# Optimization experiments

Measured on AMD Instinct MI355X. Metric: run time of the kernel, lower is better.

The kernel has to match this reference:

```python
import jax, jax.numpy as jnp
import numpy as np
from jax import lax

B, T, H, C = 64, 512, 1024, 8


def setup_inputs() -> dict:
    key = jax.random.key(0)
    ks = jax.random.split(key, 7)
    encoding = jax.random.normal(ks[0], (B, T, H), dtype=jnp.float32)
    labels = jax.random.randint(ks[1], (B, 3 * T), 0, C)
    W = jax.random.normal(ks[2], (3, C, H), dtype=jnp.float32) * 0.02
    b = jax.random.normal(ks[3], (3, C), dtype=jnp.float32) * 0.02
    start_trans = jax.random.normal(ks[4], (3, C), dtype=jnp.float32) * 0.1
    end_trans = jax.random.normal(ks[5], (3, C), dtype=jnp.float32) * 0.1
    trans = jax.random.normal(ks[6], (3, C, C), dtype=jnp.float32) * 0.1
    return {"encoding": encoding, "labels": labels, "W": W, "b": b,
            "start_trans": start_trans, "end_trans": end_trans, "trans": trans}


def crf_neg_log_lik(em, tags, start, end, trans):
    # em [B,T,C], tags [B,T] -> scalar (torchcrf reduction='sum', loss = -llh)
    bsz = em.shape[0]
    # numerator: score of gold path
    em_sc = jnp.take_along_axis(em, tags[:, :, None], axis=2)[..., 0].sum(axis=1)
    tr_sc = trans[tags[:, :-1], tags[:, 1:]].sum(axis=1)
    num = start[tags[:, 0]] + em_sc + tr_sc + end[tags[:, -1]]
    # denominator: forward algorithm (log partition)
    a0 = start[None, :] + em[:, 0]  # [B,C]

    def step(a, e_t):
        a_new = jax.nn.logsumexp(a[:, :, None] + trans[None] + e_t[:, None, :], axis=1)
        return a_new, None

    aT, _ = lax.scan(step, a0, jnp.moveaxis(em[:, 1:], 1, 0))
    logZ = jax.nn.logsumexp(aT + end[None, :], axis=1)
    return -(num - logZ).sum()


def viterbi(em, start, end, trans):
    # em [B,T,C] -> best tag path [B,T] (no mask: all sequences full length)
    v0 = start[None, :] + em[:, 0]

    def step(v, e_t):
        s = v[:, :, None] + trans[None]          # [B,C_prev,C_cur]
        bp = jnp.argmax(s, axis=1)               # [B,C]
        return jnp.max(s, axis=1) + e_t, bp

    vT, bps = lax.scan(step, v0, jnp.moveaxis(em[:, 1:], 1, 0))  # bps [T-1,B,C]
    last = jnp.argmax(vT + end[None, :], axis=1)  # [B]

    def back(tag, bp):
        prev = jnp.take_along_axis(bp, tag[:, None], axis=1)[:, 0]
        return prev, prev

    _, rev = lax.scan(back, last, bps, reverse=True)  # [T-1,B], tags for t=0..T-2
    tags = jnp.concatenate([rev, last[None]], axis=0)  # [T,B]
    return tags.T


def reference(encoding, labels, W, b, start_trans, end_trans, trans):
    # three per-task projections: logits [3,B,T,C]
    logits = jnp.einsum('bth,kch->kbtc', encoding, W) + b[:, None, None, :]
    tags = jnp.stack(jnp.split(labels, 3, axis=1))  # [3,B,T] (task/process/material)
    losses = jax.vmap(crf_neg_log_lik)(logits, tags, start_trans, end_trans, trans)
    loss = losses.sum()
    pred = jax.vmap(viterbi)(logits, start_trans, end_trans, trans)  # [3,B,T]
    return loss, logits, pred
```

## Files before the change

kernel.cpp:

```cpp
#include <hip/hip_runtime.h>

#define NB 64
#define NT 512
#define NH 1024
#define NC 8
#define NK 3
#define BT (NB*NT)
#define LOGITS_N (NK*BT*NC)

typedef unsigned short ushort;
typedef unsigned int uint;
typedef __attribute__((ext_vector_type(8))) short short8v;
typedef __attribute__((ext_vector_type(4))) float float4v;
union S8 { short8v v; ushort u[8]; };

#define QP1  0xB1
#define QP2  0x4E
#define ROR4 0x124
#define ROR8 0x128
#define HM   0x141

template<int CTRL>
__device__ __forceinline__ float dppf(float x) {
  return __int_as_float(__builtin_amdgcn_update_dpp(0, __float_as_int(x), CTRL, 0xF, 0xF, true));
}
template<int CTRL>
__device__ __forceinline__ int dppi(int x) {
  return __builtin_amdgcn_update_dpp(0, x, CTRL, 0xF, 0xF, true);
}

__device__ __forceinline__ void gload_lds16(const void* g, void* l) {
  __builtin_amdgcn_global_load_lds(
      (const __attribute__((address_space(1))) void*)g,
      (__attribute__((address_space(3))) void*)l, 16, 0, 0);
}

__global__ __launch_bounds__(256) void init_kernel(const float* __restrict__ W,
                                                   ushort* __restrict__ WB,
                                                   float* __restrict__ out) {
  const int i = blockIdx.x * 256 + threadIdx.x;
  const int ci = i >> 11;
  const int rem = i & 2047;
  const int q = rem >> 9;
  const int l = (rem >> 3) & 63;
  const int e = i & 7;
  const int k = ci * 64 + (q >> 1) * 32 + ((l >> 4) << 3) + e;
  const int j = (q & 1) * 16 + (l & 15);
  float v = 0.0f;
  if (j < 24) v = W[(j >> 3) * (NC * NH) + (j & 7) * NH + k];
  const uint b = __float_as_uint(v);
  const ushort h1 = (ushort)(b >> 16);
  const float f1 = __uint_as_float(b & 0xFFFF0000u);
  const float r1 = v - f1;
  const uint b2 = __float_as_uint(r1);
  const ushort h2 = (ushort)(b2 >> 16);
  const float f2 = __uint_as_float(b2 & 0xFFFF0000u);
  const float r2 = r1 - f2;
  const ushort h3 = (ushort)(__float_as_uint(r2) >> 16);
  WB[i] = h1;
  WB[32768 + i] = h2;
  WB[65536 + i] = h3;
  if (i == 0) out[0] = 0.0f;
}

__global__ __launch_bounds__(256, 2) void proj_kernel(const float* __restrict__ enc,
                                                      const ushort* __restrict__ WB,
                                                      const float* __restrict__ bias,
                                                      float* __restrict__ out) {
  __shared__ float  sA[2][4096];
  __shared__ ushort sB[2][6144];
  const int tid = threadIdx.x;
  const int lane = tid & 63;
  const int w = tid >> 6;
  const int row0 = blockIdx.x * 64;
  const int chrot = blockIdx.x & 15;
  const float* eb = enc + (size_t)row0 * 1024;

  float4v acc0 = {0.0f, 0.0f, 0.0f, 0.0f};
  float4v acc1 = {0.0f, 0.0f, 0.0f, 0.0f};

  auto stageA = [&](int cx, int buf) {
#pragma unroll
    for (int i = 0; i < 4; ++i) {
      const int rbase = w * 16 + i * 4;
      const int r = rbase + (lane >> 4);
      const int s = (lane & 15) ^ (r & 15);
      gload_lds16(eb + (size_t)r * 1024 + cx * 64 + s * 4, &sA[buf][rbase * 64]);
    }
  };
  auto stageB = [&](int cx, int buf) {
#pragma unroll
    for (int i = 0; i < 3; ++i) {
      const int u = i * 4 + w;
      gload_lds16(WB + i * 32768 + cx * 2048 + w * 512 + lane * 8,
                  &sB[buf][u * 512]);
    }
  };

  auto compute = [&](int buf) {
    const float* ar = &sA[buf][(w * 16 + (lane & 15)) * 64];
    const ushort* sBf = &sB[buf][0];
    const int rx = lane & 15;
    const int g = lane >> 4;
#pragma unroll
    for (int kkb = 0; kkb < 2; ++kkb) {
      const int s0 = kkb * 8 + g * 2;
      const float4 e0 = *(const float4*)&ar[(s0 ^ rx) * 4];
      const float4 e1 = *(const float4*)&ar[((s0 + 1) ^ rx) * 4];
      S8 a1, a2, a3;
      const float vals[8] = {e0.x, e0.y, e0.z, e0.w, e1.x, e1.y, e1.z, e1.w};
#pragma unroll
      for (int t = 0; t < 8; ++t) {
        const float v = vals[t];
        const uint b = __float_as_uint(v);
        a1.u[t] = (ushort)(b >> 16);
        const float f1 = __uint_as_float(b & 0xFFFF0000u);
        const float r1 = v - f1;
        const uint b2 = __float_as_uint(r1);
        a2.u[t] = (ushort)(b2 >> 16);
        const float f2 = __uint_as_float(b2 & 0xFFFF0000u);
        const float r2 = r1 - f2;
        a3.u[t] = (ushort)(__float_as_uint(r2) >> 16);
      }
#pragma unroll
      for (int jt = 0; jt < 2; ++jt) {
        const int q = kkb * 2 + jt;
        const short8v w1 = *(const short8v*)&sBf[0 * 2048 + q * 512 + lane * 8];
        const short8v w2 = *(const short8v*)&sBf[1 * 2048 + q * 512 + lane * 8];
        const short8v w3 = *(const short8v*)&sBf[2 * 2048 + q * 512 + lane * 8];
        float4v acc = jt ? acc1 : acc0;
        acc = __builtin_amdgcn_mfma_f32_16x16x32_bf16(a1.v, w1, acc, 0, 0, 0);
        acc = __builtin_amdgcn_mfma_f32_16x16x32_bf16(a2.v, w1, acc, 0, 0, 0);
        acc = __builtin_amdgcn_mfma_f32_16x16x32_bf16(a1.v, w2, acc, 0, 0, 0);
        acc = __builtin_amdgcn_mfma_f32_16x16x32_bf16(a2.v, w2, acc, 0, 0, 0);
        acc = __builtin_amdgcn_mfma_f32_16x16x32_bf16(a3.v, w1, acc, 0, 0, 0);
        acc = __builtin_amdgcn_mfma_f32_16x16x32_bf16(a1.v, w3, acc, 0, 0, 0);
        if (jt) acc1 = acc; else acc0 = acc;
      }
    }
  };

  stageA(chrot, 0);
  stageB(chrot, 0);
  __syncthreads();

#pragma unroll 1
  for (int t = 0; t < 16; ++t) {
    const int buf = t & 1;
    if (t < 15) {
      const int cx = (t + 1) ^ chrot;
      stageA(cx, buf ^ 1);
      stageB(cx, buf ^ 1);
    }
    compute(buf);
    __syncthreads();
  }

  const int g = lane >> 4, cx2 = lane & 15;
#pragma unroll
  for (int jt = 0; jt < 2; ++jt) {
    const int j = jt * 16 + cx2;
    if (j < 24) {
      const float bj = bias[j];
      const float4v acc = jt ? acc1 : acc0;
      float* ob = out + 1 + (size_t)(j >> 3) * (BT * 8) + (j & 7);
#pragma unroll
      for (int qq = 0; qq < 4; ++qq) {
        const int grow = row0 + w * 16 + g * 4 + qq;
        ob[(size_t)grow * 8] = acc[qq] + bj;
      }
    }
  }
}

__global__ __launch_bounds__(512) void crf_kernel(const int* __restrict__ labels,
                                                  const float* __restrict__ startT,
                                                  const float* __restrict__ endT,
                                                  const float* __restrict__ trans,
                                                  float* __restrict__ d_out) {
  __shared__ float sA[32 * 64];
  __shared__ float sVB[32 * 8];
  __shared__ int   sBP[512];
  __shared__ int   sMap[32 * 8];
  __shared__ int   sEnt[32];
  __shared__ float sRed[32];
  __shared__ unsigned char sTags[512];
  __shared__ int sTerm;

  const int tid = threadIdx.x;
  const int lane = tid & 63;
  const int w = tid >> 6;
  const int c = lane & 7;
  const int p = (lane >> 3) & 7;
  const int role = (blockIdx.x >= 192);
  const int seq = role ? blockIdx.x - 192 : blockIdx.x;
  const int k = seq >> 6, b = seq & 63;
  const float* em = d_out + 1 + ((size_t)k * BT + (size_t)b * 512) * 8;
  const float* trk = trans + k * 64;
  const int* lab = labels + b * (NK * NT) + k * NT;

  float Txc[8];
#pragma unroll
  for (int kk = 0; kk < 8; ++kk) Txc[kk] = trk[(c ^ kk) * 8 + c];
  const float Tpc = trk[p * 8 + c];
  const float startc = startT[k * 8 + c];
  const float endc = endT[k * 8 + c];

  if (!role) {
    float Mxc[8];
#pragma unroll
    for (int kk = 0; kk < 8; ++kk) Mxc[kk] = __expf(Txc[kk]);

#pragma unroll 1
    for (int it = 0; it < 4; ++it) {
      const int i = w * 4 + it;
      const int t0 = i * 16;
      const int te = (t0 + 16 < 512) ? (t0 + 16) : 511;
      float EX[16];
      EX[0] = em[(t0 + 1) * 8 + c];
#pragma unroll
      for (int j = 1; j < 16; ++j) {
        int t = t0 + 1 + j;
        EX[j] = (t <= te) ? __expf(em[t * 8 + c]) : 1.0f;
      }
      float V = __expf(Tpc + EX[0]);
#pragma unroll
      for (int j = 1; j < 16; ++j) {
        int t = t0 + 1 + j;
        if (t <= te) {
          float x1 = dppf<QP1>(V), x2 = dppf<QP2>(V), x3 = dppf<QP2>(x1);
          float x7 = dppf<HM>(V), x6 = dppf<QP1>(x7), x5 = dppf<QP2>(x7), x4 = dppf<QP2>(x6);
          float s01 = fmaf(x1, Mxc[1], V * Mxc[0]);
          float s23 = fmaf(x3, Mxc[3], x2 * Mxc[2]);
          float s45 = fmaf(x5, Mxc[5], x4 * Mxc[4]);
          float s67 = fmaf(x7, Mxc[7], x6 * Mxc[6]);
          V = ((s01 + s23) + (s45 + s67)) * EX[j];
        }
        if (j == 8) V *= 0x1p-32f;
      }
      sA[i * 64 + lane] = V;
    }
    __syncthreads();

    float logZ = 0.0f;
    if (w == 0) {
      float al = __expf(startc + em[c]);
      float lz = 0.0f;
#pragma unroll 1
      for (int i = 0; i < 32; ++i) {
        const float* Ai = &sA[i * 64];
        float A0 = Ai[(c ^ 0) * 8 + c], A1 = Ai[(c ^ 1) * 8 + c];
        float A2 = Ai[(c ^ 2) * 8 + c], A3 = Ai[(c ^ 3) * 8 + c];
        float A4 = Ai[(c ^ 4) * 8 + c], A5 = Ai[(c ^ 5) * 8 + c];
        float A6 = Ai[(c ^ 6) * 8 + c], A7 = Ai[(c ^ 7) * 8 + c];
        float a1 = dppf<QP1>(al), a2 = dppf<QP2>(al), a3 = dppf<QP2>(a1);
        float a4 = dppf<ROR4>(al), a5 = dppf<ROR4>(a1), a6 = dppf<ROR4>(a2), a7 = dppf<ROR4>(a3);
        float s01 = fmaf(a1, A1, al * A0);
        float s23 = fmaf(a3, A3, a2 * A2);
        float s45 = fmaf(a5, A5, a4 * A4);
        float s67 = fmaf(a7, A7, a6 * A6);
        float s = (s01 + s23) + (s45 + s67);
        float ss = s;
        ss += dppf<QP1>(ss); ss += dppf<QP2>(ss); ss += dppf<ROR4>(ss);
        lz += __logf(ss);
        al = s * (1.0f / ss);
      }
      float se = al * __expf(endc);
      se += dppf<QP1>(se); se += dppf<QP2>(se); se += dppf<ROR4>(se);
      logZ = lz + __logf(se) + 1024.0f * 0.69314718055994531f;
    } else {
      int idx = (w - 1) * 64 + lane;
      float ns = 0.0f;
      {
        int tg = lab[idx];
        ns += em[(size_t)idx * 8 + tg] + trk[tg * 8 + lab[idx + 1]];
      }
      if (idx < 64) {
        int t = idx + 448;
        int tg = lab[t];
        ns += em[(size_t)t * 8 + tg];
        if (t < 511) ns += trk[tg * 8 + lab[t + 1]];
      }
      ns += dppf<QP1>(ns); ns += dppf<QP2>(ns); ns += dppf<HM>(ns); ns += dppf<ROR8>(ns);
      if ((lane & 15) == 0) sRed[(w - 1) * 4 + (lane >> 4)] = ns;
    }
    __syncthreads();
    if (tid == 0) {
      float num = startT[k * 8 + lab[0]] + endT[k * 8 + lab[511]];
#pragma unroll
      for (int u = 0; u < 28; ++u) num += sRed[u];
      atomicAdd(d_out, logZ - num);
    }
  } else {
#pragma unroll 1
    for (int it = 0; it < 4; ++it) {
      const int i = w * 4 + it;
      const int t0 = i * 16;
      const int te = (t0 + 16 < 512) ? (t0 + 16) : 511;
      float emv[16];
#pragma unroll
      for (int j = 0; j < 16; ++j) {
        int t = t0 + 1 + j;
        emv[j] = (t <= te) ? em[t * 8 + c] : 0.0f;
      }
      float V = Tpc + emv[0];
#pragma unroll
      for (int j = 1; j < 16; ++j) {
        int t = t0 + 1 + j;
        if (t <= te) {
          float x1 = dppf<QP1>(V), x2 = dppf<QP2>(V), x3 = dppf<QP2>(x1);
          float x7 = dppf<HM>(V), x6 = dppf<QP1>(x7), x5 = dppf<QP2>(x7), x4 = dppf<QP2>(x6);
          float c0 = V + Txc[0], c1 = x1 + Txc[1], c2 = x2 + Txc[2], c3 = x3 + Txc[3];
          float c4 = x4 + Txc[4], c5 = x5 + Txc[5], c6 = x6 + Txc[6], c7 = x7 + Txc[7];
          float m0 = fmaxf(fmaxf(c0, c1), c2);
          float m1 = fmaxf(fmaxf(c3, c4), c5);
          float m2 = fmaxf(c6, c7);
          V = fmaxf(fmaxf(m0, m1), m2) + emv[j];
        }
      }
      sA[i * 64 + lane] = V;
    }
    __syncthreads();

    if (w == 0) {
      float v = startc + em[c];
#pragma unroll 1
      for (int i = 0; i < 32; ++i) {
        if (lane < 8) sVB[i * 8 + c] = v;
        const float* Ai = &sA[i * 64];
        float A0 = Ai[(c ^ 0) * 8 + c], A1 = Ai[(c ^ 1) * 8 + c];
        float A2 = Ai[(c ^ 2) * 8 + c], A3 = Ai[(c ^ 3) * 8 + c];
        float A4 = Ai[(c ^ 4) * 8 + c], A5 = Ai[(c ^ 5) * 8 + c];
        float A6 = Ai[(c ^ 6) * 8 + c], A7 = Ai[(c ^ 7) * 8 + c];
        float a1 = dppf<QP1>(v), a2 = dppf<QP2>(v), a3 = dppf<QP2>(a1);
        float a4 = dppf<ROR4>(v), a5 = dppf<ROR4>(a1), a6 = dppf<ROR4>(a2), a7 = dppf<ROR4>(a3);
        float c0 = v + A0, c1 = a1 + A1, c2 = a2 + A2, c3 = a3 + A3;
        float c4 = a4 + A4, c5 = a5 + A5, c6 = a6 + A6, c7 = a7 + A7;
        float m0 = fmaxf(fmaxf(c0, c1), c2);
        float m1 = fmaxf(fmaxf(c3, c4), c5);
        float m2 = fmaxf(c6, c7);
        v = fmaxf(fmaxf(m0, m1), m2);
      }
      float lv = v + endc;
      int li = c;
      {
        float ov; int oi; bool take;
        ov = dppf<QP1>(lv); oi = dppi<QP1>(li);
        take = (ov > lv) || (ov == lv && oi < li); lv = take ? ov : lv; li = take ? oi : li;
        ov = dppf<QP2>(lv); oi = dppi<QP2>(li);
        take = (ov > lv) || (ov == lv && oi < li); lv = take ? ov : lv; li = take ? oi : li;
        ov = dppf<ROR4>(lv); oi = dppi<ROR4>(li);
        take = (ov > lv) || (ov == lv && oi < li); lv = take ? ov : lv; li = take ? oi : li;
      }
      if (lane == 0) sTerm = li;
    }
    __syncthreads();

    if (w < 4) {
      const int u = lane >> 3;
      const int i = w * 8 + u;
      const int t0 = i * 16;
      const int te = (t0 + 16 < 512) ? (t0 + 16) : 511;
      float emv[16];
#pragma unroll
      for (int j = 0; j < 16; ++j) {
        int t = t0 + 1 + j;
        emv[j] = (t <= te) ? em[t * 8 + c] : 0.0f;
      }
      float v = sVB[i * 8 + c];
#pragma unroll
      for (int j = 0; j < 16; ++j) {
        int t = t0 + 1 + j;
        if (t <= te) {
          float x1 = dppf<QP1>(v), x2 = dppf<QP2>(v), x3 = dppf<QP2>(x1);
          float x7 = dppf<HM>(v), x6 = dppf<QP1>(x7), x5 = dppf<QP2>(x7), x4 = dppf<QP2>(x6);
          float c0 = v + Txc[0], c1 = x1 + Txc[1], c2 = x2 + Txc[2], c3 = x3 + Txc[3];
          float c4 = x4 + Txc[4], c5 = x5 + Txc[5], c6 = x6 + Txc[6], c7 = x7 + Txc[7];
          float m0 = fmaxf(fmaxf(c0, c1), c2);
          float m1 = fmaxf(fmaxf(c3, c4), c5);
          float m2 = fmaxf(c6, c7);
          float best = fmaxf(fmaxf(m0, m1), m2);
          int a0 = (c0 == best) ? (c ^ 0) : 8;
          int a1i = (c1 == best) ? (c ^ 1) : 8;
          int a2i = (c2 == best) ? (c ^ 2) : 8;
          int a3i = (c3 == best) ? (c ^ 3) : 8;
          int a4i = (c4 == best) ? (c ^ 4) : 8;
          int a5i = (c5 == best) ? (c ^ 5) : 8;
          int a6i = (c6 == best) ? (c ^ 6) : 8;
          int a7i = (c7 == best) ? (c ^ 7) : 8;
          int arg = min(min(min(a0, a1i), min(a2i, a3i)),
                        min(min(a4i, a5i), min(a6i, a7i)));
          v = best + emv[j];
          int wd = arg << (3 * c);
          wd |= dppi<QP1>(wd); wd |= dppi<QP2>(wd); wd |= dppi<HM>(wd);
          if ((lane & 7) == 0) sBP[t] = wd;
        }
      }
    }
    __syncthreads();

    if (w < 4) {
      const int u = lane >> 3;
      const int i = w * 8 + u;
      const int t0 = i * 16;
      const int te = (t0 + 16 < 512) ? (t0 + 16) : 511;
      int tag = c;
#pragma unroll
      for (int j = 16; j >= 1; --j) {
        int t = t0 + j;
        if (t <= te) tag = (sBP[t] >> (3 * tag)) & 7;
      }
      sMap[i * 8 + c] = tag;
    }
    __syncthreads();
    if (tid == 0) {
      int cur = sTerm;
#pragma unroll 1
      for (int i = 31; i >= 0; --i) { cur = sMap[i * 8 + cur]; sEnt[i] = cur; }
    }
    __syncthreads();
    if (w == 0 && lane < 32) {
      const int i = lane;
      const int t0 = i * 16;
      const int te = (t0 + 16 < 512) ? (t0 + 16) : 511;
      int tag = (i == 31) ? sTerm : sEnt[i + 1];
      if (i == 31) sTags[511] = (unsigned char)tag;
#pragma unroll
      for (int j = 16; j >= 1; --j) {
        int t = t0 + j;
        if (t <= te) { tag = (sBP[t] >> (3 * tag)) & 7; sTags[t - 1] = (unsigned char)tag; }
      }
    }
    __syncthreads();
    float* outp = d_out + 1 + LOGITS_N + (size_t)seq * 512;
    outp[tid] = (float)sTags[tid];
  }
}

extern "C" void kernel_launch(void* const* d_in, const int* in_sizes, int n_in,
                              void* d_out, int out_size, void* d_ws, size_t ws_size,
                              hipStream_t stream) {
  const float* enc    = (const float*)d_in[0];
  const int*   labels = (const int*)  d_in[1];
  const float* W      = (const float*)d_in[2];
  const float* bias   = (const float*)d_in[3];
  const float* startT = (const float*)d_in[4];
  const float* endT   = (const float*)d_in[5];
  const float* trans  = (const float*)d_in[6];
  float* out = (float*)d_out;
  ushort* WB = (ushort*)d_ws;

  init_kernel<<<dim3(128), dim3(256), 0, stream>>>(W, WB, out);
  proj_kernel<<<dim3(512), dim3(256), 0, stream>>>(enc, WB, bias, out);
  crf_kernel<<<dim3(384), dim3(512), 0, stream>>>(labels, startT, endT, trans, out);
}
```

Before: 227.3 us.

## Triple-buffer encoding tiles and use counted vmcnt waits for deeper prefetch

The projection kernel's encoding tile staging moves from double to triple buffering, so A loads run two iterations ahead while weight tiles stay one ahead. Full __syncthreads waits are replaced by explicit s_waitcnt vmcnt counts plus raw barriers, so only the loads needed for the current tile must land before compute starts. This aims to hide more global-load latency behind the MFMA work. In exchange it uses more LDS per block (which may affect the two-blocks-per-CU target) and depends on hand-counted outstanding-load numbers being correct.

```diff
diff --git a/kernel.cpp b/kernel.cpp
--- a/kernel.cpp
+++ b/kernel.cpp
@@ -67,7 +67,7 @@
                                                       const ushort* __restrict__ WB,
                                                       const float* __restrict__ bias,
                                                       float* __restrict__ out) {
-  __shared__ float  sA[2][4096];
+  __shared__ float  sA[3][4096];
   __shared__ ushort sB[2][6144];
   const int tid = threadIdx.x;
   const int lane = tid & 63;
@@ -79,27 +79,31 @@
   float4v acc0 = {0.0f, 0.0f, 0.0f, 0.0f};
   float4v acc1 = {0.0f, 0.0f, 0.0f, 0.0f};
 
-  auto stageA = [&](int cx, int buf) {
+  auto stageA = [&](int t) {
+    const int cx = t ^ chrot;
+    float* dst = &sA[t % 3][0];
 #pragma unroll
     for (int i = 0; i < 4; ++i) {
       const int rbase = w * 16 + i * 4;
       const int r = rbase + (lane >> 4);
       const int s = (lane & 15) ^ (r & 15);
-      gload_lds16(eb + (size_t)r * 1024 + cx * 64 + s * 4, &sA[buf][rbase * 64]);
+      gload_lds16(eb + (size_t)r * 1024 + cx * 64 + s * 4, &dst[rbase * 64]);
     }
   };
-  auto stageB = [&](int cx, int buf) {
+  auto stageB = [&](int t) {
+    const int cx = t ^ chrot;
+    ushort* dst = &sB[t & 1][0];
 #pragma unroll
     for (int i = 0; i < 3; ++i) {
       const int u = i * 4 + w;
       gload_lds16(WB + i * 32768 + cx * 2048 + w * 512 + lane * 8,
-                  &sB[buf][u * 512]);
+                  &dst[u * 512]);
     }
   };
 
-  auto compute = [&](int buf) {
-    const float* ar = &sA[buf][(w * 16 + (lane & 15)) * 64];
-    const ushort* sBf = &sB[buf][0];
+  auto compute = [&](int abuf, int bbuf) {
+    const float* ar = &sA[abuf][(w * 16 + (lane & 15)) * 64];
+    const ushort* sBf = &sB[bbuf][0];
     const int rx = lane & 15;
     const int g = lane >> 4;
 #pragma unroll
@@ -140,20 +144,22 @@
     }
   };
 
-  stageA(chrot, 0);
-  stageB(chrot, 0);
-  __syncthreads();
+  stageA(0);
+  stageB(0);
+  stageA(1);
 
 #pragma unroll 1
   for (int t = 0; t < 16; ++t) {
-    const int buf = t & 1;
-    if (t < 15) {
-      const int cx = (t + 1) ^ chrot;
-      stageA(cx, buf ^ 1);
-      stageB(cx, buf ^ 1);
-    }
-    compute(buf);
-    __syncthreads();
+    if (t + 1 < 16) stageB(t + 1);
+    if (t + 2 < 16) stageA(t + 2);
+    if (t < 14)       asm volatile("s_waitcnt vmcnt(11)" ::: "memory");
+    else if (t == 14) asm volatile("s_waitcnt vmcnt(7)" ::: "memory");
+    else              asm volatile("s_waitcnt vmcnt(0)" ::: "memory");
+    __builtin_amdgcn_s_barrier();
+    asm volatile("" ::: "memory");
+    compute(t % 3, t & 1);
+    asm volatile("" ::: "memory");
+    __builtin_amdgcn_s_barrier();
   }
 
   const int g = lane >> 4, cx2 = lane & 15;
```

New measurement: 226.2 us. Within noise of the previous version (-0.5%).

## Split K across waves in projection kernel with register-resident weight fragments

Applied to the files above, without the earlier changes.

The projection kernel now gives each wave a quarter of the K dimension for all 64 rows. Before, each wave owned 16 rows over the full K. Each wave holds its 12 bf16 weight fragments in registers and reuses them across four row groups. Weights are staged once per K-quarter instead of once per 64-column chunk. Partial accumulators are reduced across waves through shared memory before the bias add and store. This adds registers for four accumulator pairs and an LDS reduction epilogue, which may lower occupancy, and it drops the per-block chunk rotation.

```diff
diff --git a/kernel.cpp b/kernel.cpp
--- a/kernel.cpp
+++ b/kernel.cpp
@@ -67,107 +67,134 @@
                                                       const ushort* __restrict__ WB,
                                                       const float* __restrict__ bias,
                                                       float* __restrict__ out) {
-  __shared__ float  sA[2][4096];
-  __shared__ ushort sB[2][6144];
+  __shared__ float smem[20480];
+  float* const sAf = smem;
+  ushort* const sBu = (ushort*)(smem + 8192);
   const int tid = threadIdx.x;
   const int lane = tid & 63;
   const int w = tid >> 6;
   const int row0 = blockIdx.x * 64;
-  const int chrot = blockIdx.x & 15;
   const float* eb = enc + (size_t)row0 * 1024;
 
-  float4v acc0 = {0.0f, 0.0f, 0.0f, 0.0f};
-  float4v acc1 = {0.0f, 0.0f, 0.0f, 0.0f};
-
-  auto stageA = [&](int cx, int buf) {
+  float4v acc[4][2];
+#pragma unroll
+  for (int rg = 0; rg < 4; ++rg)
+#pragma unroll
+    for (int jt = 0; jt < 2; ++jt) acc[rg][jt] = (float4v){0.f, 0.f, 0.f, 0.f};
+
+  auto stageA = [&](int kqN, int rgN, int bufN) {
 #pragma unroll
     for (int i = 0; i < 4; ++i) {
-      const int rbase = w * 16 + i * 4;
-      const int r = rbase + (lane >> 4);
-      const int s = (lane & 15) ^ (r & 15);
-      gload_lds16(eb + (size_t)r * 1024 + cx * 64 + s * 4, &sA[buf][rbase * 64]);
+      const int r = w * 4 + i;
+      gload_lds16(eb + (size_t)(rgN * 16 + r) * 1024 + kqN * 256 + (lane ^ r) * 4,
+                  &sAf[bufN * 4096 + r * 256]);
     }
   };
-  auto stageB = [&](int cx, int buf) {
-#pragma unroll
-    for (int i = 0; i < 3; ++i) {
-      const int u = i * 4 + w;
-      gload_lds16(WB + i * 32768 + cx * 2048 + w * 512 + lane * 8,
-                  &sB[buf][u * 512]);
+  auto stageB = [&](int kqN) {
+    const int ci = kqN * 4 + w;
+#pragma unroll
+    for (int i = 0; i < 12; ++i) {
+      const int sp = i >> 2, q = i & 3;
+      gload_lds16(WB + sp * 32768 + ci * 2048 + q * 512 + lane * 8,
+                  &sBu[w * 6144 + sp * 2048 + q * 512]);
     }
   };
 
-  auto compute = [&](int buf) {
-    const float* ar = &sA[buf][(w * 16 + (lane & 15)) * 64];
-    const ushort* sBf = &sB[buf][0];
-    const int rx = lane & 15;
-    const int g = lane >> 4;
-#pragma unroll
-    for (int kkb = 0; kkb < 2; ++kkb) {
-      const int s0 = kkb * 8 + g * 2;
-      const float4 e0 = *(const float4*)&ar[(s0 ^ rx) * 4];
-      const float4 e1 = *(const float4*)&ar[((s0 + 1) ^ rx) * 4];
-      S8 a1, a2, a3;
-      const float vals[8] = {e0.x, e0.y, e0.z, e0.w, e1.x, e1.y, e1.z, e1.w};
-#pragma unroll
-      for (int t = 0; t < 8; ++t) {
-        const float v = vals[t];
-        const uint b = __float_as_uint(v);
-        a1.u[t] = (ushort)(b >> 16);
-        const float f1 = __uint_as_float(b & 0xFFFF0000u);
-        const float r1 = v - f1;
-        const uint b2 = __float_as_uint(r1);
-        a2.u[t] = (ushort)(b2 >> 16);
-        const float f2 = __uint_as_float(b2 & 0xFFFF0000u);
-        const float r2 = r1 - f2;
-        a3.u[t] = (ushort)(__float_as_uint(r2) >> 16);
-      }
-#pragma unroll
-      for (int jt = 0; jt < 2; ++jt) {
-        const int q = kkb * 2 + jt;
-        const short8v w1 = *(const short8v*)&sBf[0 * 2048 + q * 512 + lane * 8];
-        const short8v w2 = *(const short8v*)&sBf[1 * 2048 + q * 512 + lane * 8];
-        const short8v w3 = *(const short8v*)&sBf[2 * 2048 + q * 512 + lane * 8];
-        float4v acc = jt ? acc1 : acc0;
-        acc = __builtin_amdgcn_mfma_f32_16x16x32_bf16(a1.v, w1, acc, 0, 0, 0);
-        acc = __builtin_amdgcn_mfma_f32_16x16x32_bf16(a2.v, w1, acc, 0, 0, 0);
-        acc = __builtin_amdgcn_mfma_f32_16x16x32_bf16(a1.v, w2, acc, 0, 0, 0);
-        acc = __builtin_amdgcn_mfma_f32_16x16x32_bf16(a2.v, w2, acc, 0, 0, 0);
-        acc = __builtin_amdgcn_mfma_f32_16x16x32_bf16(a3.v, w1, acc, 0, 0, 0);
-        acc = __builtin_amdgcn_mfma_f32_16x16x32_bf16(a1.v, w3, acc, 0, 0, 0);
-        if (jt) acc1 = acc; else acc0 = acc;
-      }
-    }
-  };
-
-  stageA(chrot, 0);
-  stageB(chrot, 0);
+  stageB(0);
+  stageA(0, 0, 0);
   __syncthreads();
 
 #pragma unroll 1
-  for (int t = 0; t < 16; ++t) {
-    const int buf = t & 1;
-    if (t < 15) {
-      const int cx = (t + 1) ^ chrot;
-      stageA(cx, buf ^ 1);
-      stageB(cx, buf ^ 1);
-    }
-    compute(buf);
-    __syncthreads();
+  for (int kq = 0; kq < 4; ++kq) {
+#pragma unroll
+    for (int rg = 0; rg < 4; ++rg) {
+      const int buf = rg & 1;
+      if (!(kq == 3 && rg == 3)) {
+        const int rgN = (rg + 1) & 3;
+        const int kqN = kq + ((rg + 1) >> 2);
+        stageA(kqN, rgN, rgN & 1);
+      }
+      const ushort* bw = &sBu[w * 6144];
+      short8v Bf0q0 = *(const short8v*)&bw[0 * 2048 + 0 * 512 + lane * 8];
+      short8v Bf0q1 = *(const short8v*)&bw[0 * 2048 + 1 * 512 + lane * 8];
+      short8v Bf0q2 = *(const short8v*)&bw[0 * 2048 + 2 * 512 + lane * 8];
+      short8v Bf0q3 = *(const short8v*)&bw[0 * 2048 + 3 * 512 + lane * 8];
+      short8v Bf1q0 = *(const short8v*)&bw[1 * 2048 + 0 * 512 + lane * 8];
+      short8v Bf1q1 = *(const short8v*)&bw[1 * 2048 + 1 * 512 + lane * 8];
+      short8v Bf1q2 = *(const short8v*)&bw[1 * 2048 + 2 * 512 + lane * 8];
+      short8v Bf1q3 = *(const short8v*)&bw[1 * 2048 + 3 * 512 + lane * 8];
+      short8v Bf2q0 = *(const short8v*)&bw[2 * 2048 + 0 * 512 + lane * 8];
+      short8v Bf2q1 = *(const short8v*)&bw[2 * 2048 + 1 * 512 + lane * 8];
+      short8v Bf2q2 = *(const short8v*)&bw[2 * 2048 + 2 * 512 + lane * 8];
+      short8v Bf2q3 = *(const short8v*)&bw[2 * 2048 + 3 * 512 + lane * 8];
+      if (rg == 3 && kq < 3) {
+        __builtin_amdgcn_sched_barrier(0);
+        asm volatile("s_waitcnt lgkmcnt(0)" ::: "memory");
+        stageB(kq + 1);
+        __builtin_amdgcn_sched_barrier(0);
+      }
+      const int r = lane & 15;
+      const int g = lane >> 4;
+      const float* er = &sAf[buf * 4096 + r * 256];
+#pragma unroll
+      for (int kkb = 0; kkb < 2; ++kkb) {
+        const int v = w * 16 + kkb * 8 + g * 2;
+        const float4 e0 = *(const float4*)&er[(v ^ r) * 4];
+        const float4 e1 = *(const float4*)&er[((v + 1) ^ r) * 4];
+        S8 a1, a2, a3;
+        const float vals[8] = {e0.x, e0.y, e0.z, e0.w, e1.x, e1.y, e1.z, e1.w};
+#pragma unroll
+        for (int t = 0; t < 8; ++t) {
+          const float vv = vals[t];
+          const uint b = __float_as_uint(vv);
+          a1.u[t] = (ushort)(b >> 16);
+          const float p1 = __uint_as_float(b & 0xFFFF0000u);
+          const float r1 = vv - p1;
+          const uint b2 = __float_as_uint(r1);
+          a2.u[t] = (ushort)(b2 >> 16);
+          const float p2 = __uint_as_float(b2 & 0xFFFF0000u);
+          const float r2 = r1 - p2;
+          a3.u[t] = (ushort)(__float_as_uint(r2) >> 16);
+        }
+#pragma unroll
+        for (int jt = 0; jt < 2; ++jt) {
+          const short8v w1 = (kkb == 0) ? (jt == 0 ? Bf0q0 : Bf0q1) : (jt == 0 ? Bf0q2 : Bf0q3);
+          const short8v w2 = (kkb == 0) ? (jt == 0 ? Bf1q0 : Bf1q1) : (jt == 0 ? Bf1q2 : Bf1q3);
+          const short8v w3 = (kkb == 0) ? (jt == 0 ? Bf2q0 : Bf2q1) : (jt == 0 ? Bf2q2 : Bf2q3);
+          float4v a = acc[rg][jt];
+          a = __builtin_amdgcn_mfma_f32_16x16x32_bf16(a1.v, w1, a, 0, 0, 0);
+          a = __builtin_amdgcn_mfma_f32_16x16x32_bf16(a2.v, w1, a, 0, 0, 0);
+          a = __builtin_amdgcn_mfma_f32_16x16x32_bf16(a1.v, w2, a, 0, 0, 0);
+          a = __builtin_amdgcn_mfma_f32_16x16x32_bf16(a2.v, w2, a, 0, 0, 0);
+          a = __builtin_amdgcn_mfma_f32_16x16x32_bf16(a3.v, w1, a, 0, 0, 0);
+          a = __builtin_amdgcn_mfma_f32_16x16x32_bf16(a1.v, w3, a, 0, 0, 0);
+          acc[rg][jt] = a;
+        }
+      }
+      __syncthreads();
+    }
   }
 
-  const int g = lane >> 4, cx2 = lane & 15;
-#pragma unroll
-  for (int jt = 0; jt < 2; ++jt) {
-    const int j = jt * 16 + cx2;
-    if (j < 24) {
-      const float bj = bias[j];
-      const float4v acc = jt ? acc1 : acc0;
-      float* ob = out + 1 + (size_t)(j >> 3) * (BT * 8) + (j & 7);
-#pragma unroll
-      for (int qq = 0; qq < 4; ++qq) {
-        const int grow = row0 + w * 16 + g * 4 + qq;
-        ob[(size_t)grow * 8] = acc[qq] + bj;
+#pragma unroll
+  for (int rg = 0; rg < 4; ++rg) {
+    float* pw = &smem[rg * 2048 + (w * 64 + lane) * 8];
+    *(float4v*)&pw[0] = acc[rg][0];
+    *(float4v*)&pw[4] = acc[rg][1];
+  }
+  __syncthreads();
+#pragma unroll
+  for (int rg = 0; rg < 4; ++rg) {
+#pragma unroll
+    for (int rep = 0; rep < 2; ++rep) {
+      const int idx = rep * 256 + tid;
+      if (idx < 384) {
+        const int j = idx >> 4, r = idx & 15;
+        const int lane_src = (j < 16 ? j : j - 16) + ((r >> 2) << 4);
+        const int fi = (j < 16 ? 0 : 4) + (r & 3);
+        float ssum = bias[j];
+#pragma unroll
+        for (int ww = 0; ww < 4; ++ww) ssum += smem[rg * 2048 + (ww * 64 + lane_src) * 8 + fi];
+        out[1 + (size_t)(j >> 3) * (BT * 8) + (size_t)(row0 + rg * 16 + r) * 8 + (j & 7)] = ssum;
       }
     }
   }
```

New measurement: 230.5 us. No clear change (+1.4%).
